# Kernel optimization log

Hardware: AMD Instinct MI355X
Metric: run time of the kernel (lower is better)

The kernel has to match this reference:

```python
import jax, jax.numpy as jnp
import numpy as np

E_MAX = 8192  # fixed pad for the data-dependent edge count (jit-safe)
N_HITS = 8192


def setup_inputs() -> dict:
    key = jax.random.key(0)
    k1, k2, k3, k4, k5 = jax.random.split(key, 5)
    # columns: [event, x, y, z, station, track]
    r = jax.random.uniform(k1, (N_HITS,), minval=270.0, maxval=580.0)
    phi = jax.random.uniform(k2, (N_HITS,), minval=-3.1, maxval=3.1)
    # original uses phi = atan2(x, y), so x = r*sin(phi), y = r*cos(phi)
    x = r * jnp.sin(phi)
    y = r * jnp.cos(phi)
    z = jax.random.uniform(k3, (N_HITS,), minval=-2000.0, maxval=2000.0)
    station = jax.random.randint(k4, (N_HITS,), 0, 32).astype(jnp.float32)
    track = jax.random.randint(k5, (N_HITS,), 0, 1024).astype(jnp.float32)
    ev = jnp.zeros((N_HITS,), jnp.float32)  # single event -> one output graph
    event_data = jnp.stack([ev, x, y, z, station, track], axis=1)
    return {"event_data": event_data}


def _convert_normalize(event_data):
    # convert(): cartesian -> (r, phi, z); note atan2(x, y) as in the source
    x, y, z = event_data[:, 1], event_data[:, 2], event_data[:, 3]
    r = jnp.sqrt(x * x + y * y)
    phi = jnp.arctan2(x, y)
    # normalize() with hard-coded constraints [[269,581],[-3.15,3.15],[-2386,2386]]
    rn = 2.0 * (r - 269.0) / (581.0 - 269.0) - 1.0
    phin = 2.0 * (phi + 3.15) / (2.0 * 3.15) - 1.0
    zn = 2.0 * (z + 2386.0) / (2.0 * 2386.0) - 1.0
    return rn, phin, zn


def reference(event_data):
    rn, phin, zn = _convert_normalize(event_data)
    ev = event_data[:, 0].astype(jnp.int32)
    st = event_data[:, 4].astype(jnp.int32)
    # pair (i, j) valid iff same event and station_j == station_i + 1
    pair = (ev[:, None] == ev[None, :]) & (st[:, None] == (st[None, :] - 1))
    # merged[:, -2] = phi_j - phi_i ; merged[:, -1] = z_j - z_i (normalized coords)
    dphi = phin[None, :] - phin[:, None]  # [N, N]
    dz = zn[None, :] - zn[:, None]        # [N, N]
    valid = pair & (dphi > -0.04) & (dphi < 0.04) & (dz > -0.03) & (dz < 0.03)
    # torch.nonzero equivalent, padded to E_MAX (row-major order matches torch)
    src, dst = jnp.nonzero(valid, size=E_MAX, fill_value=0)
    count = jnp.sum(valid)
    edge_mask = jnp.arange(E_MAX) < count  # True for real edges, False for pads

    track = event_data[:, 5]
    # edges[:, [index_prev, index_current]] = track ids of (prev hit, next hit)
    edges = jnp.stack([track[src], track[dst]], axis=1)  # [E_MAX, 2]
    X = jnp.stack([rn, phin, zn], axis=1)  # hits[:, [1,2,3]] / 1.0
    # Ri/Ro: incidence via broadcast equality of track ids, as in the source
    Ri = ((track[:, None] == edges[None, :, 1]) & edge_mask[None, :]).astype(jnp.int32)
    Ro = ((track[:, None] == edges[None, :, 0]) & edge_mask[None, :]).astype(jnp.int32)
    y_lbl = jnp.zeros((E_MAX,), jnp.float32)
    return X, Ri, Ro, y_lbl, edges, edge_mask
```

## Files before the change

kernel.cpp:

```cpp
#include <hip/hip_runtime.h>

#define N_HITS 8192
#define E_MAX  8192
#define NSTA   32
#define NCHUNK 128

typedef float v4f __attribute__((ext_vector_type(4)));

#define WS_HITA    0
#define WS_HTRACK  131072
#define WS_CAND    163840
#define WS_CCNT    294912
#define WS_COFF    311296
#define WS_BSTART  327680
#define WS_RCNT    327840
#define WS_ROFF    360608
#define WS_TOTAL   393376
#define WS_RIQ     393472
#define WS_ROQ     426240

#define OFF_X  0
#define OFF_RI 24576
#define OFF_RO 67133440
#define OFF_Y  134242304
#define OFF_E  134250496
#define OFF_M  134266880

__global__ void k_pre(const float* __restrict__ ed, float* __restrict__ out,
                      float4* __restrict__ hitA, float* __restrict__ htrack) {
    int h = blockIdx.x * blockDim.x + threadIdx.x;
    if (h >= N_HITS) return;
    const float* row = ed + h * 6;
    float ev = row[0], x = row[1], y = row[2], z = row[3], st = row[4], tr = row[5];
    float r   = sqrtf(x * x + y * y);
    float phi = atan2f(x, y);
    float rn   = 2.0f * (r   - 269.0f)  / 312.0f  - 1.0f;
    float phin = 2.0f * (phi + 3.15f)   / 6.3f    - 1.0f;
    float zn   = 2.0f * (z   + 2386.0f) / 4772.0f - 1.0f;
    out[OFF_X + h * 3 + 0] = rn;
    out[OFF_X + h * 3 + 1] = phin;
    out[OFF_X + h * 3 + 2] = zn;
    out[OFF_Y + h] = 0.0f;
    hitA[h] = make_float4(phin, zn, (float)(int)ev, (float)(int)st);
    htrack[h] = tr;
}

__global__ void k_hist(const float4* __restrict__ hitA, int* __restrict__ ccnt) {
    int tid = threadIdx.x;
    int lane = tid & 63;
    int w = blockIdx.x * (blockDim.x >> 6) + (tid >> 6);
    int h = w * 64 + lane;
    int st = (int)hitA[h].w;
    for (int b = 0; b < NSTA; ++b) {
        unsigned long long m = __ballot(st == b);
        if (lane == 0) ccnt[b * NCHUNK + w] = __popcll(m);
    }
}

__global__ void k_scan_chunks(const int* __restrict__ cnt, int* __restrict__ off,
                              int* __restrict__ bstart) {
    __shared__ int sums[256];
    int tid = threadIdx.x;
    int base = tid * 16;
    int loc[16]; int s = 0;
    for (int k = 0; k < 16; ++k) { loc[k] = cnt[base + k]; s += loc[k]; }
    sums[tid] = s; __syncthreads();
    for (int d = 1; d < 256; d <<= 1) {
        int v = (tid >= d) ? sums[tid - d] : 0;
        __syncthreads();
        sums[tid] += v;
        __syncthreads();
    }
    int run = sums[tid] - s;
    for (int k = 0; k < 16; ++k) { off[base + k] = run; run += loc[k]; }
    __syncthreads();
    if (tid < NSTA) bstart[tid] = off[tid * NCHUNK];
    if (tid == 0)   bstart[NSTA] = N_HITS;
}

__global__ void k_scatter(const float4* __restrict__ hitA, const float* __restrict__ htrack,
                          const int* __restrict__ coff, float4* __restrict__ cand) {
    int tid = threadIdx.x;
    int lane = tid & 63;
    int w = blockIdx.x * (blockDim.x >> 6) + (tid >> 6);
    int h = w * 64 + lane;
    float4 a = hitA[h];
    float tr = htrack[h];
    int st = (int)a.w;
    for (int b = 0; b < NSTA; ++b) {
        unsigned long long m = __ballot(st == b);
        if (st == b) {
            int rank = __popcll(m & ((1ull << lane) - 1ull));
            cand[coff[b * NCHUNK + w] + rank] = make_float4(a.x, a.y, a.z, tr);
        }
    }
}

__device__ __forceinline__ bool edge_pred(float4 me, float4 cj) {
    float dphi = cj.x - me.x;
    float dz   = cj.y - me.y;
    return (cj.z == me.z) & (dphi > -0.04f) & (dphi < 0.04f)
                          & (dz > -0.03f) & (dz < 0.03f);
}

__global__ void k_rowcount(const float4* __restrict__ hitA, const float4* __restrict__ cand,
                           const int* __restrict__ bstart, int* __restrict__ rcnt) {
    int tid = threadIdx.x;
    int lane = tid & 63;
    int row = blockIdx.x * (blockDim.x >> 6) + (tid >> 6);
    float4 me = hitA[row];
    int b = (int)me.w + 1;
    int cnt = 0;
    if (b >= 1 && b < NSTA) {
        int s = bstart[b], e = bstart[b + 1];
        for (int k0 = s; k0 < e; k0 += 64) {
            int kk = k0 + lane;
            bool p = false;
            if (kk < e) p = edge_pred(me, cand[kk]);
            cnt += __popcll(__ballot(p));
        }
    }
    if (lane == 0) rcnt[row] = cnt;
}

__global__ void k_scan_rows(const int* __restrict__ cnt, int* __restrict__ off,
                            int* __restrict__ total) {
    __shared__ int sums[256];
    int tid = threadIdx.x;
    int base = tid * 32;
    int loc[32]; int s = 0;
    for (int k = 0; k < 32; ++k) { loc[k] = cnt[base + k]; s += loc[k]; }
    sums[tid] = s; __syncthreads();
    for (int d = 1; d < 256; d <<= 1) {
        int v = (tid >= d) ? sums[tid - d] : 0;
        __syncthreads();
        sums[tid] += v;
        __syncthreads();
    }
    int run = sums[tid] - s;
    for (int k = 0; k < 32; ++k) { off[base + k] = run; run += loc[k]; }
    if (tid == 255) *total = sums[255];
}

__global__ void k_emit(const float4* __restrict__ hitA, const float* __restrict__ htrack,
                       const float4* __restrict__ cand, const int* __restrict__ bstart,
                       const int* __restrict__ roff, float* __restrict__ riq,
                       float* __restrict__ roq, float* __restrict__ out) {
    int tid = threadIdx.x;
    int lane = tid & 63;
    int row = blockIdx.x * (blockDim.x >> 6) + (tid >> 6);
    float4 me = hitA[row];
    int b = (int)me.w + 1;
    if (b < 1 || b >= NSTA) return;
    float tr_i = htrack[row];
    int s = bstart[b], e = bstart[b + 1];
    int base = roff[row];
    int c = 0;
    for (int k0 = s; k0 < e; k0 += 64) {
        int kk = k0 + lane;
        float4 cj = make_float4(0.f, 0.f, 0.f, 0.f);
        bool p = false;
        if (kk < e) { cj = cand[kk]; p = edge_pred(me, cj); }
        unsigned long long m = __ballot(p);
        if (p) {
            int idx = base + c + __popcll(m & ((1ull << lane) - 1ull));
            if (idx < E_MAX) {
                riq[idx] = cj.w;
                roq[idx] = tr_i;
                out[OFF_E + 2 * idx]     = tr_i;
                out[OFF_E + 2 * idx + 1] = cj.w;
            }
        }
        c += __popcll(m);
    }
}

__global__ void k_pad(const int* __restrict__ total, const float* __restrict__ htrack,
                      float* __restrict__ riq, float* __restrict__ roq,
                      float* __restrict__ out) {
    int e = blockIdx.x * blockDim.x + threadIdx.x;
    if (e >= E_MAX) return;
    int S = *total;
    bool valid = e < S;
    out[OFF_M + e] = valid ? 1.0f : 0.0f;
    if (!valid) {
        float t0 = htrack[0];
        out[OFF_E + 2 * e]     = t0;
        out[OFF_E + 2 * e + 1] = t0;
        riq[e] = -1.0f;
        roq[e] = -1.0f;
    }
}

__global__ void __launch_bounds__(256) k_big(const float* __restrict__ htrack,
                                             const float* __restrict__ riq,
                                             const float* __restrict__ roq,
                                             float* __restrict__ out) {
    int h  = blockIdx.y;
    int e4 = blockIdx.x * 256 + threadIdx.x;
    float t = htrack[h];
    const v4f* riq4 = (const v4f*)riq;
    const v4f* roq4 = (const v4f*)roq;
    v4f a = riq4[e4];
    v4f b = roq4[e4];
    v4f ri, ro;
    ri.x = (t == a.x) ? 1.f : 0.f; ri.y = (t == a.y) ? 1.f : 0.f;
    ri.z = (t == a.z) ? 1.f : 0.f; ri.w = (t == a.w) ? 1.f : 0.f;
    ro.x = (t == b.x) ? 1.f : 0.f; ro.y = (t == b.y) ? 1.f : 0.f;
    ro.z = (t == b.z) ? 1.f : 0.f; ro.w = (t == b.w) ? 1.f : 0.f;
    size_t off = (size_t)h * 2048 + e4;
    __builtin_nontemporal_store(ri, (v4f*)(out + OFF_RI) + off);
    __builtin_nontemporal_store(ro, (v4f*)(out + OFF_RO) + off);
}

extern "C" void kernel_launch(void* const* d_in, const int* in_sizes, int n_in,
                              void* d_out, int out_size, void* d_ws, size_t ws_size,
                              hipStream_t stream) {
    const float* ed = (const float*)d_in[0];
    float* out = (float*)d_out;
    char* ws = (char*)d_ws;

    float4* hitA   = (float4*)(ws + WS_HITA);
    float*  htrack = (float*) (ws + WS_HTRACK);
    float4* cand   = (float4*)(ws + WS_CAND);
    int*    ccnt   = (int*)   (ws + WS_CCNT);
    int*    coff   = (int*)   (ws + WS_COFF);
    int*    bstart = (int*)   (ws + WS_BSTART);
    int*    rcnt   = (int*)   (ws + WS_RCNT);
    int*    roffp  = (int*)   (ws + WS_ROFF);
    int*    total  = (int*)   (ws + WS_TOTAL);
    float*  riq    = (float*) (ws + WS_RIQ);
    float*  roq    = (float*) (ws + WS_ROQ);

    hipLaunchKernelGGL(k_pre,        dim3(32),   dim3(256), 0, stream, ed, out, hitA, htrack);
    hipLaunchKernelGGL(k_hist,       dim3(32),   dim3(256), 0, stream, hitA, ccnt);
    hipLaunchKernelGGL(k_scan_chunks,dim3(1),    dim3(256), 0, stream, ccnt, coff, bstart);
    hipLaunchKernelGGL(k_scatter,    dim3(32),   dim3(256), 0, stream, hitA, htrack, coff, cand);
    hipLaunchKernelGGL(k_rowcount,   dim3(2048), dim3(256), 0, stream, hitA, cand, bstart, rcnt);
    hipLaunchKernelGGL(k_scan_rows,  dim3(1),    dim3(256), 0, stream, rcnt, roffp, total);
    hipLaunchKernelGGL(k_emit,       dim3(2048), dim3(256), 0, stream, hitA, htrack, cand, bstart, roffp, riq, roq, out);
    hipLaunchKernelGGL(k_pad,        dim3(32),   dim3(256), 0, stream, total, htrack, riq, roq, out);
    hipLaunchKernelGGL(k_big,        dim3(8, 8192), dim3(256), 0, stream, htrack, riq, roq, out);
}
```

Before: 544.4 us.

## Replace dense Ri/Ro comparison pass with memset plus sparse scatter via track buckets

Drops the dense k_big pass, which compared every hit track against every edge endpoint over the full 8192x8192 Ri and Ro matrices. Instead it memsets Ri/Ro to zero, buckets hits by track id (counting, scan, fill), and has k_emit scatter 1.0 only at hits whose track matches each edge endpoint. It also fuses the histogram into k_pre, merges the two scans, and folds padding into the row scan to cut launches. The memset still writes the full 512MB, so the saving is mainly the loads and compares. The atomic bucket fill is nondeterministic in order, and the y_lbl zeroing is dropped from k_pre, though the memset range covers it.

New measurement: 556.4 us. 1.02x slower.

```diff
diff --git a/kernel.cpp b/kernel.cpp
--- a/kernel.cpp
+++ b/kernel.cpp
@@ -3,9 +3,8 @@
 #define N_HITS 8192
 #define E_MAX  8192
 #define NSTA   32
+#define NTRK   1024
 #define NCHUNK 128
-
-typedef float v4f __attribute__((ext_vector_type(4)));
 
 #define WS_HITA    0
 #define WS_HTRACK  131072
@@ -13,11 +12,12 @@
 #define WS_CCNT    294912
 #define WS_COFF    311296
 #define WS_BSTART  327680
-#define WS_RCNT    327840
-#define WS_ROFF    360608
-#define WS_TOTAL   393376
-#define WS_RIQ     393472
-#define WS_ROQ     426240
+#define WS_RCNT    327936
+#define WS_ROFF    360704
+#define WS_TCNT    393472
+#define WS_TFILL   397568
+#define WS_TOFF    401664
+#define WS_THITS   405760
 
 #define OFF_X  0
 #define OFF_RI 24576
@@ -27,11 +27,13 @@
 #define OFF_M  134266880
 
 __global__ void k_pre(const float* __restrict__ ed, float* __restrict__ out,
-                      float4* __restrict__ hitA, float* __restrict__ htrack) {
+                      float4* __restrict__ hitA, float* __restrict__ htrack,
+                      int* __restrict__ ccnt, int* __restrict__ tcnt) {
     int h = blockIdx.x * blockDim.x + threadIdx.x;
-    if (h >= N_HITS) return;
+    int lane = threadIdx.x & 63;
+    int w = h >> 6;
     const float* row = ed + h * 6;
-    float ev = row[0], x = row[1], y = row[2], z = row[3], st = row[4], tr = row[5];
+    float ev = row[0], x = row[1], y = row[2], z = row[3], stf = row[4], tr = row[5];
     float r   = sqrtf(x * x + y * y);
     float phi = atan2f(x, y);
     float rn   = 2.0f * (r   - 269.0f)  / 312.0f  - 1.0f;
@@ -40,50 +42,62 @@
     out[OFF_X + h * 3 + 0] = rn;
     out[OFF_X + h * 3 + 1] = phin;
     out[OFF_X + h * 3 + 2] = zn;
-    out[OFF_Y + h] = 0.0f;
-    hitA[h] = make_float4(phin, zn, (float)(int)ev, (float)(int)st);
+    int st = (int)stf;
+    hitA[h] = make_float4(phin, zn, (float)(int)ev, stf);
     htrack[h] = tr;
-}
-
-__global__ void k_hist(const float4* __restrict__ hitA, int* __restrict__ ccnt) {
-    int tid = threadIdx.x;
-    int lane = tid & 63;
-    int w = blockIdx.x * (blockDim.x >> 6) + (tid >> 6);
-    int h = w * 64 + lane;
-    int st = (int)hitA[h].w;
     for (int b = 0; b < NSTA; ++b) {
         unsigned long long m = __ballot(st == b);
         if (lane == 0) ccnt[b * NCHUNK + w] = __popcll(m);
     }
-}
-
-__global__ void k_scan_chunks(const int* __restrict__ cnt, int* __restrict__ off,
-                              int* __restrict__ bstart) {
+    atomicAdd(&tcnt[(int)tr], 1);
+}
+
+__global__ void k_scans(const int* __restrict__ ccnt, int* __restrict__ coff,
+                        int* __restrict__ bstart,
+                        const int* __restrict__ tcnt, int* __restrict__ toff) {
     __shared__ int sums[256];
     int tid = threadIdx.x;
-    int base = tid * 16;
-    int loc[16]; int s = 0;
-    for (int k = 0; k < 16; ++k) { loc[k] = cnt[base + k]; s += loc[k]; }
-    sums[tid] = s; __syncthreads();
-    for (int d = 1; d < 256; d <<= 1) {
-        int v = (tid >= d) ? sums[tid - d] : 0;
-        __syncthreads();
-        sums[tid] += v;
-        __syncthreads();
-    }
-    int run = sums[tid] - s;
-    for (int k = 0; k < 16; ++k) { off[base + k] = run; run += loc[k]; }
-    __syncthreads();
-    if (tid < NSTA) bstart[tid] = off[tid * NCHUNK];
-    if (tid == 0)   bstart[NSTA] = N_HITS;
+    {
+        int base = tid * 16;
+        int loc[16]; int s = 0;
+        for (int k = 0; k < 16; ++k) { loc[k] = ccnt[base + k]; s += loc[k]; }
+        sums[tid] = s; __syncthreads();
+        for (int d = 1; d < 256; d <<= 1) {
+            int v = (tid >= d) ? sums[tid - d] : 0;
+            __syncthreads();
+            sums[tid] += v;
+            __syncthreads();
+        }
+        int run = sums[tid] - s;
+        for (int k = 0; k < 16; ++k) { coff[base + k] = run; run += loc[k]; }
+        __syncthreads();
+        if (tid < NSTA) bstart[tid] = coff[tid * NCHUNK];
+        if (tid == 0)   bstart[NSTA] = N_HITS;
+        __syncthreads();
+    }
+    {
+        int base = tid * 4;
+        int loc[4]; int s = 0;
+        for (int k = 0; k < 4; ++k) { loc[k] = tcnt[base + k]; s += loc[k]; }
+        sums[tid] = s; __syncthreads();
+        for (int d = 1; d < 256; d <<= 1) {
+            int v = (tid >= d) ? sums[tid - d] : 0;
+            __syncthreads();
+            sums[tid] += v;
+            __syncthreads();
+        }
+        int run = sums[tid] - s;
+        for (int k = 0; k < 4; ++k) { toff[base + k] = run; run += loc[k]; }
+    }
 }
 
 __global__ void k_scatter(const float4* __restrict__ hitA, const float* __restrict__ htrack,
-                          const int* __restrict__ coff, float4* __restrict__ cand) {
-    int tid = threadIdx.x;
-    int lane = tid & 63;
-    int w = blockIdx.x * (blockDim.x >> 6) + (tid >> 6);
-    int h = w * 64 + lane;
+                          const int* __restrict__ coff, float4* __restrict__ cand,
+                          const int* __restrict__ toff, int* __restrict__ tfill,
+                          int* __restrict__ thits) {
+    int h = blockIdx.x * blockDim.x + threadIdx.x;
+    int lane = threadIdx.x & 63;
+    int w = h >> 6;
     float4 a = hitA[h];
     float tr = htrack[h];
     int st = (int)a.w;
@@ -94,6 +108,9 @@
             cand[coff[b * NCHUNK + w] + rank] = make_float4(a.x, a.y, a.z, tr);
         }
     }
+    int ti = (int)tr;
+    int pos = atomicAdd(&tfill[ti], 1);
+    thits[toff[ti] + pos] = h;
 }
 
 __device__ __forceinline__ bool edge_pred(float4 me, float4 cj) {
@@ -123,13 +140,13 @@
     if (lane == 0) rcnt[row] = cnt;
 }
 
-__global__ void k_scan_rows(const int* __restrict__ cnt, int* __restrict__ off,
-                            int* __restrict__ total) {
+__global__ void k_scanrows(const int* __restrict__ rcnt, int* __restrict__ roff,
+                           const float* __restrict__ htrack, float* __restrict__ out) {
     __shared__ int sums[256];
     int tid = threadIdx.x;
     int base = tid * 32;
     int loc[32]; int s = 0;
-    for (int k = 0; k < 32; ++k) { loc[k] = cnt[base + k]; s += loc[k]; }
+    for (int k = 0; k < 32; ++k) { loc[k] = rcnt[base + k]; s += loc[k]; }
     sums[tid] = s; __syncthreads();
     for (int d = 1; d < 256; d <<= 1) {
         int v = (tid >= d) ? sums[tid - d] : 0;
@@ -138,14 +155,25 @@
         __syncthreads();
     }
     int run = sums[tid] - s;
-    for (int k = 0; k < 32; ++k) { off[base + k] = run; run += loc[k]; }
-    if (tid == 255) *total = sums[255];
+    for (int k = 0; k < 32; ++k) { roff[base + k] = run; run += loc[k]; }
+    __syncthreads();
+    int S = sums[255];
+    float t0 = htrack[0];
+    for (int e = tid; e < E_MAX; e += 256) {
+        bool v = e < S;
+        out[OFF_M + e] = v ? 1.0f : 0.0f;
+        if (!v) {
+            out[OFF_E + 2 * e]     = t0;
+            out[OFF_E + 2 * e + 1] = t0;
+        }
+    }
 }
 
 __global__ void k_emit(const float4* __restrict__ hitA, const float* __restrict__ htrack,
                        const float4* __restrict__ cand, const int* __restrict__ bstart,
-                       const int* __restrict__ roff, float* __restrict__ riq,
-                       float* __restrict__ roq, float* __restrict__ out) {
+                       const int* __restrict__ roff, const int* __restrict__ toff,
+                       const int* __restrict__ tcnt, const int* __restrict__ thits,
+                       float* __restrict__ out) {
     int tid = threadIdx.x;
     int lane = tid & 63;
     int row = blockIdx.x * (blockDim.x >> 6) + (tid >> 6);
@@ -153,6 +181,8 @@
     int b = (int)me.w + 1;
     if (b < 1 || b >= NSTA) return;
     float tr_i = htrack[row];
+    int bo = (int)tr_i;
+    int os = toff[bo], oc = tcnt[bo];
     int s = bstart[b], e = bstart[b + 1];
     int base = roff[row];
     int c = 0;
@@ -165,52 +195,18 @@
         if (p) {
             int idx = base + c + __popcll(m & ((1ull << lane) - 1ull));
             if (idx < E_MAX) {
-                riq[idx] = cj.w;
-                roq[idx] = tr_i;
                 out[OFF_E + 2 * idx]     = tr_i;
                 out[OFF_E + 2 * idx + 1] = cj.w;
+                for (int j = 0; j < oc; ++j)
+                    out[OFF_RO + (size_t)thits[os + j] * E_MAX + idx] = 1.0f;
+                int bi = (int)cj.w;
+                int is = toff[bi], ic = tcnt[bi];
+                for (int j = 0; j < ic; ++j)
+                    out[OFF_RI + (size_t)thits[is + j] * E_MAX + idx] = 1.0f;
             }
         }
         c += __popcll(m);
     }
-}
-
-__global__ void k_pad(const int* __restrict__ total, const float* __restrict__ htrack,
-                      float* __restrict__ riq, float* __restrict__ roq,
-                      float* __restrict__ out) {
-    int e = blockIdx.x * blockDim.x + threadIdx.x;
-    if (e >= E_MAX) return;
-    int S = *total;
-    bool valid = e < S;
-    out[OFF_M + e] = valid ? 1.0f : 0.0f;
-    if (!valid) {
-        float t0 = htrack[0];
-        out[OFF_E + 2 * e]     = t0;
-        out[OFF_E + 2 * e + 1] = t0;
-        riq[e] = -1.0f;
-        roq[e] = -1.0f;
-    }
-}
-
-__global__ void __launch_bounds__(256) k_big(const float* __restrict__ htrack,
-                                             const float* __restrict__ riq,
-                                             const float* __restrict__ roq,
-                                             float* __restrict__ out) {
-    int h  = blockIdx.y;
-    int e4 = blockIdx.x * 256 + threadIdx.x;
-    float t = htrack[h];
-    const v4f* riq4 = (const v4f*)riq;
-    const v4f* roq4 = (const v4f*)roq;
-    v4f a = riq4[e4];
-    v4f b = roq4[e4];
-    v4f ri, ro;
-    ri.x = (t == a.x) ? 1.f : 0.f; ri.y = (t == a.y) ? 1.f : 0.f;
-    ri.z = (t == a.z) ? 1.f : 0.f; ri.w = (t == a.w) ? 1.f : 0.f;
-    ro.x = (t == b.x) ? 1.f : 0.f; ro.y = (t == b.y) ? 1.f : 0.f;
-    ro.z = (t == b.z) ? 1.f : 0.f; ro.w = (t == b.w) ? 1.f : 0.f;
-    size_t off = (size_t)h * 2048 + e4;
-    __builtin_nontemporal_store(ri, (v4f*)(out + OFF_RI) + off);
-    __builtin_nontemporal_store(ro, (v4f*)(out + OFF_RO) + off);
 }
 
 extern "C" void kernel_launch(void* const* d_in, const int* in_sizes, int n_in,
@@ -228,17 +224,18 @@
     int*    bstart = (int*)   (ws + WS_BSTART);
     int*    rcnt   = (int*)   (ws + WS_RCNT);
     int*    roffp  = (int*)   (ws + WS_ROFF);
-    int*    total  = (int*)   (ws + WS_TOTAL);
-    float*  riq    = (float*) (ws + WS_RIQ);
-    float*  roq    = (float*) (ws + WS_ROQ);
-
-    hipLaunchKernelGGL(k_pre,        dim3(32),   dim3(256), 0, stream, ed, out, hitA, htrack);
-    hipLaunchKernelGGL(k_hist,       dim3(32),   dim3(256), 0, stream, hitA, ccnt);
-    hipLaunchKernelGGL(k_scan_chunks,dim3(1),    dim3(256), 0, stream, ccnt, coff, bstart);
-    hipLaunchKernelGGL(k_scatter,    dim3(32),   dim3(256), 0, stream, hitA, htrack, coff, cand);
-    hipLaunchKernelGGL(k_rowcount,   dim3(2048), dim3(256), 0, stream, hitA, cand, bstart, rcnt);
-    hipLaunchKernelGGL(k_scan_rows,  dim3(1),    dim3(256), 0, stream, rcnt, roffp, total);
-    hipLaunchKernelGGL(k_emit,       dim3(2048), dim3(256), 0, stream, hitA, htrack, cand, bstart, roffp, riq, roq, out);
-    hipLaunchKernelGGL(k_pad,        dim3(32),   dim3(256), 0, stream, total, htrack, riq, roq, out);
-    hipLaunchKernelGGL(k_big,        dim3(8, 8192), dim3(256), 0, stream, htrack, riq, roq, out);
-}
+    int*    tcnt   = (int*)   (ws + WS_TCNT);
+    int*    tfill  = (int*)   (ws + WS_TFILL);
+    int*    toff   = (int*)   (ws + WS_TOFF);
+    int*    thits  = (int*)   (ws + WS_THITS);
+
+    hipMemsetAsync(out + OFF_RI, 0, (size_t)(OFF_E - OFF_RI) * sizeof(float), stream);
+    hipMemsetAsync(ws + WS_TCNT, 0, 2 * NTRK * sizeof(int), stream);
+
+    hipLaunchKernelGGL(k_pre,      dim3(32),   dim3(256), 0, stream, ed, out, hitA, htrack, ccnt, tcnt);
+    hipLaunchKernelGGL(k_scans,    dim3(1),    dim3(256), 0, stream, ccnt, coff, bstart, tcnt, toff);
+    hipLaunchKernelGGL(k_scatter,  dim3(32),   dim3(256), 0, stream, hitA, htrack, coff, cand, toff, tfill, thits);
+    hipLaunchKernelGGL(k_rowcount, dim3(2048), dim3(256), 0, stream, hitA, cand, bstart, rcnt);
+    hipLaunchKernelGGL(k_scanrows, dim3(1),    dim3(256), 0, stream, rcnt, roffp, htrack, out);
+    hipLaunchKernelGGL(k_emit,     dim3(2048), dim3(256), 0, stream, hitA, htrack, cand, bstart, roffp, toff, tcnt, thits, out);
+}
```
